# Performance work log

Hardware: AMD Instinct MI355X
Metric: run time of the kernel (lower is better)

## Reference

```python
import jax, jax.numpy as jnp
import numpy as np

NUM_HEADS = 16
EMBED_DIM = 1024
HEAD_DIM = EMBED_DIM // NUM_HEADS
SCALE = HEAD_DIM * -0.5  # faithful to source: multiplicative, negative


def setup_inputs() -> dict:
    key = jax.random.key(0)
    kx, kq, kk, kv, ko = jax.random.split(key, 5)
    B, S, E = 2, 2048, EMBED_DIM
    std = 1.0 / np.sqrt(E)
    return {
        "x": jax.random.normal(kx, (B, S, E), dtype=jnp.float32),
        "Wq": jax.random.normal(kq, (E, E), dtype=jnp.float32) * std,
        "Wk": jax.random.normal(kk, (E, E), dtype=jnp.float32) * std,
        "Wv": jax.random.normal(kv, (E, E), dtype=jnp.float32) * std,
        "Wo": jax.random.normal(ko, (E, E), dtype=jnp.float32) * std,
    }


def reference(x, Wq, Wk, Wv, Wo):
    B, S, E = x.shape
    H, D = NUM_HEADS, HEAD_DIM
    # nn.Linear(bias=False): y = x @ W.T
    q = (x @ Wq.T).reshape(B, S, H, D).transpose(0, 2, 1, 3)  # unused downstream (faithful to source)
    k = (x @ Wk.T).reshape(B, S, H, D).transpose(0, 2, 1, 3)  # [B,H,S,D]
    v = (x @ Wv.T).reshape(B, S, H, D).transpose(0, 2, 1, 3)
    # Source bug reproduced: logits = K @ V^T, scaled by head_dim * -0.5
    logits = jnp.einsum('bhsd,bhtd->bhst', k, v) * SCALE  # [B,H,S,S]
    attn = jax.nn.softmax(logits, axis=-1)
    out = jnp.einsum('bhst,bhtd->bhsd', attn, v)  # [B,H,S,D]
    out = out.transpose(0, 2, 1, 3).reshape(B, S, E)
    return out @ Wo.T
```

## Files before the change

### kernel.cpp

```cpp
#include <hip/hip_runtime.h>
#include <math.h>

#define B_ 2
#define S_ 2048
#define E_ 1024
#define H_ 16
#define D_ 64
#define M_ (B_ * S_)
#define SC2 (-46.166241308446828f)

typedef unsigned short u16;
typedef _Float16 f16;
typedef __attribute__((ext_vector_type(8))) _Float16 f16x8;
typedef __attribute__((ext_vector_type(2))) __fp16 fp16x2_n;
typedef __attribute__((ext_vector_type(16))) float f32x16;

static __device__ __forceinline__ f32x16 mfma_h(f16x8 a, f16x8 b, f32x16 c) {
    return __builtin_amdgcn_mfma_f32_32x32x16_f16(a, b, c, 0, 0, 0);
}
static __device__ __forceinline__ u16 f16bits(f16 h) {
    union { f16 h; u16 u; } c; c.h = h; return c.u;
}
static __device__ __forceinline__ unsigned pack2(u16 a, u16 b) {
    return (unsigned)a | ((unsigned)b << 16);
}
static __device__ __forceinline__ unsigned pkrtz(float a, float b) {
    fp16x2_n h = __builtin_amdgcn_cvt_pkrtz(a, b);
    unsigned u; __builtin_memcpy(&u, &h, 4); return u;
}
#define ROWMAP(r, hh) (((r) & 3) + ((((r) >> 2)) << 3) + ((hh) << 2))

__global__ __launch_bounds__(256)
void convert_split(const float* __restrict__ x, const float* __restrict__ Wk,
                   const float* __restrict__ Wv, const float* __restrict__ Wo,
                   u16* __restrict__ Xh, u16* __restrict__ Xl,
                   u16* __restrict__ Wkh, u16* __restrict__ Wkl,
                   u16* __restrict__ Wvh, u16* __restrict__ Wvl,
                   u16* __restrict__ Woh)
{
    const int blk = blockIdx.x;
    const float* src; u16 *dh, *dl; int base; float sc = 1.0f; bool wantlo = true;
    if (blk < 4096)      { src = x;  dh = Xh;  dl = Xl;  base = blk; }
    else if (blk < 5120) { src = Wk; dh = Wkh; dl = Wkl; base = blk - 4096; sc = SC2; }
    else if (blk < 6144) { src = Wv; dh = Wvh; dl = Wvl; base = blk - 5120; }
    else                 { src = Wo; dh = Woh; dl = Woh; base = blk - 6144; wantlo = false; }
    const size_t off = ((size_t)base * 256 + threadIdx.x) * 4;
    const float4 v = *(const float4*)(src + off);
    const float f[4] = {v.x * sc, v.y * sc, v.z * sc, v.w * sc};
    u16 h4[4], l4[4];
#pragma unroll
    for (int i = 0; i < 4; ++i) {
        const f16 h = (f16)f[i];
        h4[i] = f16bits(h);
        l4[i] = f16bits((f16)(f[i] - (float)h));
    }
    *(uint2*)(dh + off) = make_uint2(pack2(h4[0], h4[1]), pack2(h4[2], h4[3]));
    if (wantlo)
        *(uint2*)(dl + off) = make_uint2(pack2(l4[0], l4[1]), pack2(l4[2], l4[3]));
}

#define CSB 1032
#define ARR (4 * CSB)

template<int MODE>
__global__ __launch_bounds__(512, 2)
void gemm_f(const u16* __restrict__ Ah_, const u16* __restrict__ Al_,
            const u16* __restrict__ Bkh_, const u16* __restrict__ Bkl_,
            const u16* __restrict__ Bvh_, const u16* __restrict__ Bvl_,
            u16* __restrict__ Khg, u16* __restrict__ Klg,
            u16* __restrict__ Vhg, u16* __restrict__ Vtg,
            float* __restrict__ Cout)
{
    constexpr int NARR = (MODE == 0 ? 6 : 2);
    constexpr int SSZ = (NARR * ARR > 16384 ? NARR * ARR : 16384);
    __shared__ u16 stage[SSZ];

    const int tid = threadIdx.x;
    const int w = tid >> 6, l31 = tid & 31, hh = (tid >> 5) & 1;
    const int wt = w & 3, ws = w >> 2;
    const int wm = (wt >> 1) << 6, wn = (wt & 1) << 6;
    const int m0 = blockIdx.y * 128, n0 = blockIdx.x * 128;
    const int ch8 = (ws << 1) + hh;

    const int sr = tid >> 2, sch = tid & 3;
    const size_t gA = (size_t)(m0 + sr) * E_ + (sch << 3);
    const size_t gB = (size_t)(n0 + sr) * E_ + (sch << 3);
    const int slo = sch * CSB + sr * 8;

    f32x16 acc1[2][2], acc2[2][2];
#pragma unroll
    for (int mt = 0; mt < 2; ++mt)
#pragma unroll
        for (int nt = 0; nt < 2; ++nt)
#pragma unroll
            for (int r = 0; r < 16; ++r) {
                acc1[mt][nt][r] = 0.f;
                if constexpr (MODE == 0) acc2[mt][nt][r] = 0.f;
            }

    f16x8 pf[NARR];
    auto load_tile = [&](int k0) {
        pf[0] = *(const f16x8*)(Ah_ + gA + k0);
        if constexpr (MODE == 0) {
            pf[1] = *(const f16x8*)(Al_ + gA + k0);
            pf[2] = *(const f16x8*)(Bkh_ + gB + k0);
            pf[3] = *(const f16x8*)(Bkl_ + gB + k0);
            pf[4] = *(const f16x8*)(Bvh_ + gB + k0);
            pf[5] = *(const f16x8*)(Bvl_ + gB + k0);
        } else {
            pf[1] = *(const f16x8*)(Bkh_ + gB + k0);
        }
    };
    auto store_tile = [&]() {
#pragma unroll
        for (int a = 0; a < NARR; ++a)
            *(f16x8*)&stage[a * ARR + slo] = pf[a];
    };

    load_tile(0);
    for (int it = 0; it < 32; ++it) {
        store_tile();
        __syncthreads();
        if (it + 1 < 32) load_tile((it + 1) << 5);

        const int co = ch8 * CSB;
        f16x8 xh[2], xl[2];
#pragma unroll
        for (int mt = 0; mt < 2; ++mt) {
            const int off = co + (wm + (mt << 5) + l31) * 8;
            xh[mt] = *(const f16x8*)&stage[0 * ARR + off];
            if constexpr (MODE == 0)
                xl[mt] = *(const f16x8*)&stage[1 * ARR + off];
        }
#pragma unroll
        for (int nt = 0; nt < 2; ++nt) {
            const int ro = co + (wn + (nt << 5) + l31) * 8;
            if constexpr (MODE == 0) {
                const f16x8 bkh = *(const f16x8*)&stage[2 * ARR + ro];
                const f16x8 bkl = *(const f16x8*)&stage[3 * ARR + ro];
                const f16x8 bvh = *(const f16x8*)&stage[4 * ARR + ro];
                const f16x8 bvl = *(const f16x8*)&stage[5 * ARR + ro];
#pragma unroll
                for (int mt = 0; mt < 2; ++mt) {
                    acc1[mt][nt] = mfma_h(xh[mt], bkh, acc1[mt][nt]);
                    acc1[mt][nt] = mfma_h(xh[mt], bkl, acc1[mt][nt]);
                    acc1[mt][nt] = mfma_h(xl[mt], bkh, acc1[mt][nt]);
                    acc2[mt][nt] = mfma_h(xh[mt], bvh, acc2[mt][nt]);
                    acc2[mt][nt] = mfma_h(xh[mt], bvl, acc2[mt][nt]);
                    acc2[mt][nt] = mfma_h(xl[mt], bvh, acc2[mt][nt]);
                }
            } else {
                const f16x8 bh = *(const f16x8*)&stage[1 * ARR + ro];
#pragma unroll
                for (int mt = 0; mt < 2; ++mt)
                    acc1[mt][nt] = mfma_h(xh[mt], bh, acc1[mt][nt]);
            }
        }
        __syncthreads();
    }

    float* red = (float*)stage;
    constexpr int NR = (MODE == 0 ? 4 : 2);
#pragma unroll
    for (int rd = 0; rd < NR; ++rd) {
        const int mt = rd & 1;
        f32x16 (*A)[2] = (MODE == 0 && rd >= 2) ? acc2 : acc1;
        __syncthreads();
        if (ws == 1) {
#pragma unroll
            for (int nt = 0; nt < 2; ++nt)
#pragma unroll
                for (int r = 0; r < 16; ++r)
                    red[(((wt << 1) + nt) << 10) + (r << 6) + (hh << 5) + l31] = A[mt][nt][r];
        }
        __syncthreads();
        if (ws == 0) {
#pragma unroll
            for (int nt = 0; nt < 2; ++nt)
#pragma unroll
                for (int r = 0; r < 16; ++r)
                    A[mt][nt][r] += red[(((wt << 1) + nt) << 10) + (r << 6) + (hh << 5) + l31];
        }
    }
    if (ws != 0) return;

#pragma unroll
    for (int nt = 0; nt < 2; ++nt) {
        const int n = n0 + wn + (nt << 5) + l31;
        if constexpr (MODE == 1) {
#pragma unroll
            for (int mt = 0; mt < 2; ++mt)
#pragma unroll
                for (int r = 0; r < 16; ++r) {
                    const int m = m0 + wm + (mt << 5) + ROWMAP(r, hh);
                    Cout[(size_t)m * E_ + n] = acc1[mt][nt][r];
                }
        } else {
            const int hd = n >> 6, d = n & 63;
            const int b = m0 >> 11;
#pragma unroll
            for (int mt = 0; mt < 2; ++mt) {
                u16 vb16[16];
#pragma unroll
                for (int r = 0; r < 16; ++r) {
                    const int s = (m0 + wm + (mt << 5) + ROWMAP(r, hh)) & (S_ - 1);
                    const size_t ib = (((size_t)(b * H_ + hd) << 11) + s) * D_ + d;
                    const float kv = acc1[mt][nt][r];
                    const f16 kh = (f16)kv;
                    Khg[ib] = f16bits(kh);
                    Klg[ib] = f16bits((f16)(kv - (float)kh));
                    const f16 vh = (f16)acc2[mt][nt][r];
                    vb16[r] = f16bits(vh);
                    Vhg[ib] = vb16[r];
                }
                const size_t vtb = ((size_t)(b * H_ + hd) * D_ + d) << 11;
#pragma unroll
                for (int g = 0; g < 4; ++g) {
                    const int s0 = ((m0 + wm + (mt << 5)) & (S_ - 1)) + (g << 3) + (hh << 2);
                    *(uint2*)&Vtg[vtb + s0] =
                        make_uint2(pack2(vb16[4 * g], vb16[4 * g + 1]),
                                   pack2(vb16[4 * g + 2], vb16[4 * g + 3]));
                }
            }
        }
    }
}

#define CSA 520
#define VA  (8 * CSA)
#define CSP 264
#define PW  (8 * CSP)

__global__ __launch_bounds__(512, 2)
void attn_mfma(const u16* __restrict__ Kh, const u16* __restrict__ Kl,
               const u16* __restrict__ Vh, const u16* __restrict__ Vt,
               u16* __restrict__ Obuf)
{
    __shared__ u16 sV[2 * VA];
    __shared__ u16 sP[8][PW];
    __shared__ float Alpha[8][32], Linv[8][32];

    const int tid = threadIdx.x;
    const int w = tid >> 6, l31 = tid & 31, hh = (tid >> 5) & 1;
    const int bh = blockIdx.y;
    const int sbase = blockIdx.x * 256 + (w << 5);
    const int sg = sbase + l31;

    f16x8 kfh[4], kfl[4];
    {
        const size_t kb = ((size_t)bh * S_ + sg) * D_;
#pragma unroll
        for (int ks = 0; ks < 4; ++ks) {
            const int db = (ks << 4) + (hh << 3);
            kfh[ks] = *(const f16x8*)(Kh + kb + db);
            kfl[ks] = *(const f16x8*)(Kl + kb + db);
        }
    }

    f32x16 oacc[2];
#pragma unroll
    for (int r = 0; r < 16; ++r) { oacc[0][r] = 0.f; oacc[1][r] = 0.f; }
    float m_i = -INFINITY, l_i = 0.f;

    const int rr = tid >> 3, cc = tid & 7;
    const size_t gn = ((size_t)bh * S_ + rr) * D_ + (cc << 3);
    const size_t gt = ((size_t)bh * D_ + rr) * S_ + (cc << 3);
    const int slo = cc * CSA + rr * 8;
    u16* P = &sP[w][0];

    f16x8 pv[2];
    auto load_tile = [&](int t0) {
        pv[0] = *(const f16x8*)(Vh + gn + (size_t)t0 * D_);
        pv[1] = *(const f16x8*)(Vt + gt + t0);
    };

    load_tile(0);
    for (int it = 0; it < 32; ++it) {
        *(f16x8*)&sV[slo] = pv[0];
        *(f16x8*)&sV[VA + slo] = pv[1];
        __syncthreads();
        if (it + 1 < 32) load_tile((it + 1) << 6);

        f32x16 sta[2], stb[2];
#pragma unroll
        for (int r = 0; r < 16; ++r) {
            sta[0][r] = 0.f; sta[1][r] = 0.f;
            stb[0][r] = 0.f; stb[1][r] = 0.f;
        }
#pragma unroll
        for (int ks = 0; ks < 4; ++ks) {
            const int ch = (ks << 1) + hh;
#pragma unroll
            for (int mt = 0; mt < 2; ++mt) {
                const f16x8 av = *(const f16x8*)&sV[ch * CSA + ((mt << 5) + l31) * 8];
                sta[mt] = mfma_h(av, kfh[ks], sta[mt]);
                stb[mt] = mfma_h(av, kfl[ks], stb[mt]);
            }
        }
#pragma unroll
        for (int mt = 0; mt < 2; ++mt)
#pragma unroll
            for (int r = 0; r < 16; ++r) sta[mt][r] += stb[mt][r];

        float tmax = -INFINITY;
#pragma unroll
        for (int mt = 0; mt < 2; ++mt)
#pragma unroll
            for (int r = 0; r < 16; ++r) tmax = fmaxf(tmax, sta[mt][r]);
        tmax = fmaxf(tmax, __shfl_xor(tmax, 32));
        const float mnew = fmaxf(m_i, tmax);
        const float alpha = __builtin_amdgcn_exp2f(m_i - mnew);
        m_i = mnew;
        const unsigned long long cmask = __ballot(tmax >= mnew - 30.f);

        if (cmask) {
            float rsum = 0.f;
#pragma unroll
            for (int mt = 0; mt < 2; ++mt)
#pragma unroll
                for (int r = 0; r < 16; ++r) {
                    const float p = __builtin_amdgcn_exp2f(sta[mt][r] - mnew);
                    sta[mt][r] = p;
                    rsum += p;
                }
            rsum += __shfl_xor(rsum, 32);
            l_i = l_i * alpha + rsum;
        }
        if (__ballot(alpha != 1.0f)) {
            if (hh == 0) Alpha[w][l31] = alpha;
#pragma unroll
            for (int g = 0; g < 4; ++g) {
                const float4 av = *(const float4*)&Alpha[w][(g << 3) + (hh << 2)];
                const float af[4] = {av.x, av.y, av.z, av.w};
#pragma unroll
                for (int q = 0; q < 4; ++q) {
                    oacc[0][(g << 2) + q] *= af[q];
                    oacc[1][(g << 2) + q] *= af[q];
                }
            }
        }
        if (cmask) {
#pragma unroll
            for (int mt = 0; mt < 2; ++mt)
#pragma unroll
                for (int g = 0; g < 4; ++g)
                    *(uint2*)&P[((mt << 2) + g) * CSP + l31 * 8 + (hh << 2)] =
                        make_uint2(pkrtz(sta[mt][4 * g], sta[mt][4 * g + 1]),
                                   pkrtz(sta[mt][4 * g + 2], sta[mt][4 * g + 3]));
#pragma unroll
            for (int ks = 0; ks < 4; ++ks) {
                const int ch = (ks << 1) + hh;
                const f16x8 pfr = *(const f16x8*)&P[ch * CSP + l31 * 8];
#pragma unroll
                for (int nt = 0; nt < 2; ++nt) {
                    const f16x8 vtf = *(const f16x8*)&sV[VA + ch * CSA + ((nt << 5) + l31) * 8];
                    oacc[nt] = mfma_h(pfr, vtf, oacc[nt]);
                }
            }
        }
        __syncthreads();
    }

    if (hh == 0) Linv[w][l31] = 1.0f / l_i;
    const int b = bh >> 4;
    const int hd = bh & 15;
    u16* Or = Obuf + ((size_t)b * S_ + sbase) * E_ + (hd << 6);
#pragma unroll
    for (int g = 0; g < 4; ++g) {
        const float4 iv = *(const float4*)&Linv[w][(g << 3) + (hh << 2)];
        const float invs[4] = {iv.x, iv.y, iv.z, iv.w};
#pragma unroll
        for (int nt = 0; nt < 2; ++nt)
#pragma unroll
            for (int q = 0; q < 4; ++q) {
                const int sl = (g << 3) + (hh << 2) + q;
                Or[(size_t)sl * E_ + (nt << 5) + l31] =
                    f16bits((f16)(oacc[nt][(g << 2) + q] * invs[q]));
            }
    }
}

extern "C" void kernel_launch(void* const* d_in, const int* in_sizes, int n_in,
                              void* d_out, int out_size, void* d_ws, size_t ws_size,
                              hipStream_t stream)
{
    (void)in_sizes; (void)n_in; (void)out_size; (void)ws_size;
    const float* x  = (const float*)d_in[0];
    const float* Wk = (const float*)d_in[2];
    const float* Wv = (const float*)d_in[3];
    const float* Wo = (const float*)d_in[4];
    float* out = (float*)d_out;

    char* ws = (char*)d_ws;
    const size_t MB = 1u << 20;
    u16* Xh  = (u16*)(ws + 0 * MB);
    u16* Xl  = (u16*)(ws + 8 * MB);
    u16* Wkh = (u16*)(ws + 16 * MB);
    u16* Wkl = (u16*)(ws + 18 * MB);
    u16* Wvh = (u16*)(ws + 20 * MB);
    u16* Wvl = (u16*)(ws + 22 * MB);
    u16* Woh = (u16*)(ws + 24 * MB);
    u16* Kh  = (u16*)(ws + 26 * MB);
    u16* Kl  = (u16*)(ws + 34 * MB);
    u16* Vh  = (u16*)(ws + 42 * MB);
    u16* Vt  = (u16*)(ws + 50 * MB);
    u16* Obuf = Xl;

    convert_split<<<7168, 256, 0, stream>>>(x, Wk, Wv, Wo,
                                            Xh, Xl, Wkh, Wkl, Wvh, Wvl, Woh);
    gemm_f<0><<<dim3(E_ / 128, M_ / 128), 512, 0, stream>>>(
        Xh, Xl, Wkh, Wkl, Wvh, Wvl, Kh, Kl, Vh, Vt, nullptr);
    attn_mfma<<<dim3(S_ / 256, B_ * H_), 512, 0, stream>>>(Kh, Kl, Vh, Vt, Obuf);
    gemm_f<1><<<dim3(E_ / 128, M_ / 128), 512, 0, stream>>>(
        Obuf, Obuf, Woh, Woh, Woh, Woh,
        nullptr, nullptr, nullptr, nullptr, out);
}
```

Before: 221.9 us.

## Split attention key range across two blocks and merge partial outputs

Adds a split-KV (flash-decoding style) dimension to the attention grid: each block handles half of the key/value sequence and writes a normalized partial output plus its row max and sum. A new merge kernel combines the two partials with log-sum-exp weights before the output projection. This doubles the number of attention blocks from 256 to 512 to fill more CUs, and launch bounds are raised to request higher occupancy. The cost is extra global traffic for the partial outputs and stats, an additional kernel launch, and possible register pressure or spilling from the tighter launch bound.

```diff
diff --git a/kernel.cpp b/kernel.cpp
--- a/kernel.cpp
+++ b/kernel.cpp
@@ -7,6 +7,7 @@
 #define H_ 16
 #define D_ 64
 #define M_ (B_ * S_)
+#define BHS_ (B_ * H_ * S_)
 #define SC2 (-46.166241308446828f)
 
 typedef unsigned short u16;
@@ -231,10 +232,11 @@
 #define CSP 264
 #define PW  (8 * CSP)
 
-__global__ __launch_bounds__(512, 2)
+__global__ __launch_bounds__(512, 4)
 void attn_mfma(const u16* __restrict__ Kh, const u16* __restrict__ Kl,
                const u16* __restrict__ Vh, const u16* __restrict__ Vt,
-               u16* __restrict__ Obuf)
+               u16* __restrict__ O0, u16* __restrict__ O1,
+               float* __restrict__ ML)
 {
     __shared__ u16 sV[2 * VA];
     __shared__ u16 sP[8][PW];
@@ -243,6 +245,7 @@
     const int tid = threadIdx.x;
     const int w = tid >> 6, l31 = tid & 31, hh = (tid >> 5) & 1;
     const int bh = blockIdx.y;
+    const int ts = blockIdx.z;
     const int sbase = blockIdx.x * 256 + (w << 5);
     const int sg = sbase + l31;
 
@@ -269,17 +272,18 @@
     u16* P = &sP[w][0];
 
     f16x8 pv[2];
-    auto load_tile = [&](int t0) {
-        pv[0] = *(const f16x8*)(Vh + gn + (size_t)t0 * D_);
+    auto load_tile = [&](int it2) {
+        const size_t t0 = (size_t)((ts << 4) + it2) << 6;
+        pv[0] = *(const f16x8*)(Vh + gn + t0 * D_);
         pv[1] = *(const f16x8*)(Vt + gt + t0);
     };
 
     load_tile(0);
-    for (int it = 0; it < 32; ++it) {
+    for (int it = 0; it < 16; ++it) {
         *(f16x8*)&sV[slo] = pv[0];
         *(f16x8*)&sV[VA + slo] = pv[1];
         __syncthreads();
-        if (it + 1 < 32) load_tile((it + 1) << 6);
+        if (it + 1 < 16) load_tile(it + 1);
 
         f32x16 sta[2], stb[2];
 #pragma unroll
@@ -361,10 +365,17 @@
         __syncthreads();
     }
 
-    if (hh == 0) Linv[w][l31] = 1.0f / l_i;
+    if (hh == 0) Linv[w][l31] = (l_i > 0.f) ? (1.0f / l_i) : 0.f;
+    {
+        float* MLh = ML + (size_t)ts * (2 * BHS_);
+        if (hh == 0) {
+            MLh[bh * S_ + sg] = m_i;
+            MLh[BHS_ + bh * S_ + sg] = l_i;
+        }
+    }
     const int b = bh >> 4;
     const int hd = bh & 15;
-    u16* Or = Obuf + ((size_t)b * S_ + sbase) * E_ + (hd << 6);
+    u16* Or = (ts ? O1 : O0) + ((size_t)b * S_ + sbase) * E_ + (hd << 6);
 #pragma unroll
     for (int g = 0; g < 4; ++g) {
         const float4 iv = *(const float4*)&Linv[w][(g << 3) + (hh << 2)];
@@ -378,6 +389,33 @@
                     f16bits((f16)(oacc[nt][(g << 2) + q] * invs[q]));
             }
     }
+}
+
+__global__ __launch_bounds__(256)
+void merge_o(const u16* __restrict__ O0, const u16* __restrict__ O1,
+             const float* __restrict__ ML, u16* __restrict__ Obuf)
+{
+    const size_t t = (size_t)blockIdx.x * 256 + threadIdx.x;
+    const size_t o = t << 3;
+    const int row = (int)(o >> 10);
+    const int e0 = (int)(o & 1023);
+    const int b = row >> 11, s = row & (S_ - 1);
+    const int h = e0 >> 6;
+    const int idx = (((b << 4) + h) << 11) + s;
+    const float m0 = ML[idx],            l0 = ML[BHS_ + idx];
+    const float m1 = ML[2 * BHS_ + idx], l1 = ML[3 * BHS_ + idx];
+    const float mm = fmaxf(m0, m1);
+    const float w0 = l0 * __builtin_amdgcn_exp2f(m0 - mm);
+    const float w1 = l1 * __builtin_amdgcn_exp2f(m1 - mm);
+    const float inv = 1.0f / (w0 + w1);
+    const float r0 = w0 * inv, r1 = w1 * inv;
+    const f16x8 a = *(const f16x8*)(O0 + o);
+    const f16x8 c = *(const f16x8*)(O1 + o);
+    f16x8 r;
+#pragma unroll
+    for (int j = 0; j < 8; ++j)
+        r[j] = (f16)(r0 * (float)a[j] + r1 * (float)c[j]);
+    *(f16x8*)(Obuf + o) = r;
 }
 
 extern "C" void kernel_launch(void* const* d_in, const int* in_sizes, int n_in,
@@ -404,13 +442,18 @@
     u16* Kl  = (u16*)(ws + 34 * MB);
     u16* Vh  = (u16*)(ws + 42 * MB);
     u16* Vt  = (u16*)(ws + 50 * MB);
+    float* ML = (float*)(ws + 58 * MB);
+    u16* O0   = Xh;
+    u16* O1   = Wkh;
     u16* Obuf = Xl;
 
     convert_split<<<7168, 256, 0, stream>>>(x, Wk, Wv, Wo,
                                             Xh, Xl, Wkh, Wkl, Wvh, Wvl, Woh);
     gemm_f<0><<<dim3(E_ / 128, M_ / 128), 512, 0, stream>>>(
         Xh, Xl, Wkh, Wkl, Wvh, Wvl, Kh, Kl, Vh, Vt, nullptr);
-    attn_mfma<<<dim3(S_ / 256, B_ * H_), 512, 0, stream>>>(Kh, Kl, Vh, Vt, Obuf);
+    attn_mfma<<<dim3(S_ / 256, B_ * H_, 2), 512, 0, stream>>>(
+        Kh, Kl, Vh, Vt, O0, O1, ML);
+    merge_o<<<(M_ * E_ / 8) / 256, 256, 0, stream>>>(O0, O1, ML, Obuf);
     gemm_f<1><<<dim3(E_ / 128, M_ / 128), 512, 0, stream>>>(
         Obuf, Obuf, Woh, Woh, Woh, Woh,
         nullptr, nullptr, nullptr, nullptr, out);
```

Measured after the change: 272.9 us. 1.23x slower.

## Keep P in registers via permlane32 swap and double-buffer V tiles

Applied to the files above, without the earlier changes.

The attention kernel no longer stages the softmax probabilities through shared memory. It repacks them in registers with v_permlane32_swap and computes the transposed product (Vt as A operand, P as B operand), so each lane owns one query row. That removes the shared Alpha/Linv tables: the rescale by alpha and the final 1/l normalization become per-lane scalars, and outputs are written as packed 8-byte stores. V tiles are now double-buffered in LDS with one barrier per iteration, which lets the next tile's store overlap compute. The extra LDS buffer replaces the P buffer, and the alpha rescale now runs unconditionally inside the cmask branch.

```diff
diff --git a/kernel.cpp b/kernel.cpp
--- a/kernel.cpp
+++ b/kernel.cpp
@@ -27,6 +27,9 @@
 static __device__ __forceinline__ unsigned pkrtz(float a, float b) {
     fp16x2_n h = __builtin_amdgcn_cvt_pkrtz(a, b);
     unsigned u; __builtin_memcpy(&u, &h, 4); return u;
+}
+static __device__ __forceinline__ void pl32swap(unsigned &a, unsigned &b) {
+    asm volatile("v_permlane32_swap_b32 %0, %1" : "+v"(a), "+v"(b));
 }
 #define ROWMAP(r, hh) (((r) & 3) + ((((r) >> 2)) << 3) + ((hh) << 2))
 
@@ -228,17 +231,13 @@
 
 #define CSA 520
 #define VA  (8 * CSA)
-#define CSP 264
-#define PW  (8 * CSP)
 
 __global__ __launch_bounds__(512, 2)
 void attn_mfma(const u16* __restrict__ Kh, const u16* __restrict__ Kl,
                const u16* __restrict__ Vh, const u16* __restrict__ Vt,
                u16* __restrict__ Obuf)
 {
-    __shared__ u16 sV[2 * VA];
-    __shared__ u16 sP[8][PW];
-    __shared__ float Alpha[8][32], Linv[8][32];
+    __shared__ u16 sV[4 * VA];
 
     const int tid = threadIdx.x;
     const int w = tid >> 6, l31 = tid & 31, hh = (tid >> 5) & 1;
@@ -266,20 +265,23 @@
     const size_t gn = ((size_t)bh * S_ + rr) * D_ + (cc << 3);
     const size_t gt = ((size_t)bh * D_ + rr) * S_ + (cc << 3);
     const int slo = cc * CSA + rr * 8;
-    u16* P = &sP[w][0];
 
     f16x8 pv[2];
-    auto load_tile = [&](int t0) {
-        pv[0] = *(const f16x8*)(Vh + gn + (size_t)t0 * D_);
+    auto load_tile = [&](int it2) {
+        const size_t t0 = (size_t)it2 << 6;
+        pv[0] = *(const f16x8*)(Vh + gn + t0 * D_);
         pv[1] = *(const f16x8*)(Vt + gt + t0);
     };
 
     load_tile(0);
+    *(f16x8*)&sV[slo] = pv[0];
+    *(f16x8*)&sV[VA + slo] = pv[1];
+    __syncthreads();
+
     for (int it = 0; it < 32; ++it) {
-        *(f16x8*)&sV[slo] = pv[0];
-        *(f16x8*)&sV[VA + slo] = pv[1];
-        __syncthreads();
-        if (it + 1 < 32) load_tile((it + 1) << 6);
+        const int vb = (it & 1) * (2 * VA);
+        const int nb = ((it + 1) & 1) * (2 * VA);
+        if (it + 1 < 32) load_tile(it + 1);
 
         f32x16 sta[2], stb[2];
 #pragma unroll
@@ -292,7 +294,7 @@
             const int ch = (ks << 1) + hh;
 #pragma unroll
             for (int mt = 0; mt < 2; ++mt) {
-                const f16x8 av = *(const f16x8*)&sV[ch * CSA + ((mt << 5) + l31) * 8];
+                const f16x8 av = *(const f16x8*)&sV[vb + ch * CSA + ((mt << 5) + l31) * 8];
                 sta[mt] = mfma_h(av, kfh[ks], sta[mt]);
                 stb[mt] = mfma_h(av, kfl[ks], stb[mt]);
             }
@@ -325,59 +327,59 @@
                 }
             rsum += __shfl_xor(rsum, 32);
             l_i = l_i * alpha + rsum;
-        }
-        if (__ballot(alpha != 1.0f)) {
-            if (hh == 0) Alpha[w][l31] = alpha;
-#pragma unroll
-            for (int g = 0; g < 4; ++g) {
-                const float4 av = *(const float4*)&Alpha[w][(g << 3) + (hh << 2)];
-                const float af[4] = {av.x, av.y, av.z, av.w};
+
+#pragma unroll
+            for (int r = 0; r < 16; ++r) { oacc[0][r] *= alpha; oacc[1][r] *= alpha; }
+
+            unsigned pa[2][4], pb[2][4];
+#pragma unroll
+            for (int mt = 0; mt < 2; ++mt)
 #pragma unroll
                 for (int q = 0; q < 4; ++q) {
-                    oacc[0][(g << 2) + q] *= af[q];
-                    oacc[1][(g << 2) + q] *= af[q];
+                    pa[mt][q] = pkrtz(sta[mt][4 * q + 0], sta[mt][4 * q + 1]);
+                    pb[mt][q] = pkrtz(sta[mt][4 * q + 2], sta[mt][4 * q + 3]);
+                }
+
+#pragma unroll
+            for (int ks = 0; ks < 4; ++ks) {
+                const int mt = ks >> 1, kk = ks & 1;
+                unsigned w0 = pa[mt][2 * kk], w2v = pa[mt][2 * kk + 1];
+                pl32swap(w0, w2v);
+                unsigned w1 = pb[mt][2 * kk], w3v = pb[mt][2 * kk + 1];
+                pl32swap(w1, w3v);
+                union { unsigned u[4]; f16x8 v; } bw;
+                bw.u[0] = w0; bw.u[1] = w1; bw.u[2] = w2v; bw.u[3] = w3v;
+                const int ch = (ks << 1) + hh;
+#pragma unroll
+                for (int nt = 0; nt < 2; ++nt) {
+                    const f16x8 vtf = *(const f16x8*)&sV[vb + VA + ch * CSA + ((nt << 5) + l31) * 8];
+                    oacc[nt] = mfma_h(vtf, bw.v, oacc[nt]);
                 }
             }
         }
-        if (cmask) {
-#pragma unroll
-            for (int mt = 0; mt < 2; ++mt)
-#pragma unroll
-                for (int g = 0; g < 4; ++g)
-                    *(uint2*)&P[((mt << 2) + g) * CSP + l31 * 8 + (hh << 2)] =
-                        make_uint2(pkrtz(sta[mt][4 * g], sta[mt][4 * g + 1]),
-                                   pkrtz(sta[mt][4 * g + 2], sta[mt][4 * g + 3]));
-#pragma unroll
-            for (int ks = 0; ks < 4; ++ks) {
-                const int ch = (ks << 1) + hh;
-                const f16x8 pfr = *(const f16x8*)&P[ch * CSP + l31 * 8];
-#pragma unroll
-                for (int nt = 0; nt < 2; ++nt) {
-                    const f16x8 vtf = *(const f16x8*)&sV[VA + ch * CSA + ((nt << 5) + l31) * 8];
-                    oacc[nt] = mfma_h(pfr, vtf, oacc[nt]);
-                }
-            }
+
+        if (it + 1 < 32) {
+            *(f16x8*)&sV[nb + slo] = pv[0];
+            *(f16x8*)&sV[nb + VA + slo] = pv[1];
         }
         __syncthreads();
     }
 
-    if (hh == 0) Linv[w][l31] = 1.0f / l_i;
+    const float linv = (l_i > 0.f) ? (1.0f / l_i) : 0.f;
     const int b = bh >> 4;
     const int hd = bh & 15;
-    u16* Or = Obuf + ((size_t)b * S_ + sbase) * E_ + (hd << 6);
-#pragma unroll
-    for (int g = 0; g < 4; ++g) {
-        const float4 iv = *(const float4*)&Linv[w][(g << 3) + (hh << 2)];
-        const float invs[4] = {iv.x, iv.y, iv.z, iv.w};
-#pragma unroll
-        for (int nt = 0; nt < 2; ++nt)
-#pragma unroll
-            for (int q = 0; q < 4; ++q) {
-                const int sl = (g << 3) + (hh << 2) + q;
-                Or[(size_t)sl * E_ + (nt << 5) + l31] =
-                    f16bits((f16)(oacc[nt][(g << 2) + q] * invs[q]));
-            }
-    }
+    u16* Or = Obuf + ((size_t)b * S_ + sg) * E_ + (hd << 6);
+#pragma unroll
+    for (int nt = 0; nt < 2; ++nt)
+#pragma unroll
+        for (int q = 0; q < 4; ++q) {
+            const int d0 = (nt << 5) + (q << 3) + (hh << 2);
+            u16 c[4];
+#pragma unroll
+            for (int j = 0; j < 4; ++j)
+                c[j] = f16bits((f16)(oacc[nt][4 * q + j] * linv));
+            *(uint2*)&Or[d0] = make_uint2(pack2(c[0], c[1]), pack2(c[2], c[3]));
+        }
 }
 
 extern "C" void kernel_launch(void* const* d_in, const int* in_sizes, int n_in,
```

Result: no change. 218.7 us (-1.4%).
